# Kernel tuning notes

Measured on AMD Instinct MI355X. Metric: run time of the kernel, lower is better.

## Reference

```python
import jax, jax.numpy as jnp
import numpy as np

N, E, B = 50000, 600000, 64


def setup_inputs() -> dict:
    key = jax.random.key(0)
    ks = jax.random.split(key, 24)
    gn = lambda k, shape, s=0.1: jax.random.normal(k, shape, dtype=jnp.float32) * s
    return {
        "x": gn(ks[0], (N, 1), 1.0),
        "edge_index": jax.random.randint(ks[1], (2, E), 0, N),
        "batch": jnp.sort(jax.random.randint(ks[2], (N,), 0, B)),
        # GATConv(1,128)
        "W1": gn(ks[3], (1, 128)), "a1s": gn(ks[4], (128,)), "a1d": gn(ks[5], (128,)), "b1": jnp.zeros((128,), jnp.float32),
        # GATConv(128,128) x2
        "W2": gn(ks[6], (128, 128)), "a2s": gn(ks[7], (128,)), "a2d": gn(ks[8], (128,)), "b2": jnp.zeros((128,), jnp.float32),
        "W3": gn(ks[9], (128, 128)), "a3s": gn(ks[10], (128,)), "a3d": gn(ks[11], (128,)), "b3": jnp.zeros((128,), jnp.float32),
        # GCNConv(128,64), GCNConv(64,32)
        "Wg1": gn(ks[12], (128, 64)), "bg1": jnp.zeros((64,), jnp.float32),
        "Wg2": gn(ks[13], (64, 32)), "bg2": jnp.zeros((32,), jnp.float32),
        # SoftmaxAggregation learnable temperature (init 1.0)
        "t": jnp.ones((), jnp.float32),
        # Linear heads
        "Wl1": gn(ks[14], (32, 16)), "bl1": jnp.zeros((16,), jnp.float32),
        "Wl2": gn(ks[15], (16, 2)), "bl2": jnp.zeros((2,), jnp.float32),
    }


def reference(x, edge_index, batch, W1, a1s, a1d, b1, W2, a2s, a2d, b2,
              W3, a3s, a3d, b3, Wg1, bg1, Wg2, bg2, t, Wl1, bl1, Wl2, bl2):
    # add self-loops (PyG default for GATConv and GCNConv)
    loops = jnp.arange(N)
    ei = jnp.concatenate([edge_index, jnp.stack([loops, loops])], axis=1)
    src, dst = ei[0], ei[1]  # messages flow src -> dst

    def seg_softmax(logits, seg, num):
        m = jax.ops.segment_max(logits, seg, num)
        m = jnp.where(jnp.isfinite(m), m, 0.0)
        e = jnp.exp(logits - m[seg])
        s = jax.ops.segment_sum(e, seg, num)
        return e / (s[seg] + 1e-16)

    def gat(h_in, W, a_src, a_dst, b):
        h = h_in @ W                                   # [N, F]
        logit = jax.nn.leaky_relu((h @ a_src)[src] + (h @ a_dst)[dst], 0.2)
        alpha = seg_softmax(logit, dst, N)             # edge-softmax over neighbors of dst
        return jax.ops.segment_sum(alpha[:, None] * h[src], dst, N) + b

    def gcn(h_in, W, b):
        deg = jax.ops.segment_sum(jnp.ones(src.shape[0], h_in.dtype), dst, N)
        dinv = jnp.where(deg > 0, jax.lax.rsqrt(deg), 0.0)
        norm = dinv[src] * dinv[dst]                   # symmetric normalization
        h = h_in @ W
        return jax.ops.segment_sum(norm[:, None] * h[src], dst, N) + b

    h = jax.nn.elu(gat(x, W1, a1s, a1d, b1))
    h = jax.nn.elu(gat(h, W2, a2s, a2d, b2))
    h = jax.nn.elu(gat(h, W3, a3s, a3d, b3))
    h = jax.nn.elu(gcn(h, Wg1, bg1))
    h = jax.nn.elu(gcn(h, Wg2, bg2))

    # SoftmaxAggregation: per-graph, per-channel softmax weights w = softmax(t*h)
    logits = h * t
    m = jax.ops.segment_max(logits, batch, B)
    m = jnp.where(jnp.isfinite(m), m, 0.0)
    e = jnp.exp(logits - m[batch])
    s = jax.ops.segment_sum(e, batch, B)
    w = e / (s[batch] + 1e-16)
    g = jax.ops.segment_sum(w * h, batch, B)           # [B, 32]

    g = jax.nn.elu(g @ Wl1 + bl1)
    return jax.nn.log_softmax(g @ Wl2 + bl2, axis=1)
```

## Files before the change

kernel.cpp:

```cpp
#include <hip/hip_runtime.h>
#include <math.h>

static inline int cdiv(long a, long b){ return (int)((a + b - 1) / b); }
static inline char* alignp(char* p, size_t a){ return (char*)(((uintptr_t)p + a - 1) & ~(uintptr_t)(a - 1)); }

typedef __attribute__((ext_vector_type(8))) short bf16x8;
typedef __attribute__((ext_vector_type(4))) short bf16x4;
typedef __attribute__((ext_vector_type(4))) float f32x4;

__device__ __forceinline__ float lrelu(float x){ return x > 0.f ? x : 0.2f * x; }
__device__ __forceinline__ float eluf(float x){ return x > 0.f ? x : __expf(x) - 1.f; }
__device__ __forceinline__ short f2bf(float f){
  unsigned u = __float_as_uint(f);
  return (short)((u + 0x7FFFu + ((u >> 16) & 1u)) >> 16);
}
__device__ __forceinline__ float bflo(unsigned v){ return __uint_as_float(v << 16); }
__device__ __forceinline__ float bfhi(unsigned v){ return __uint_as_float(v & 0xFFFF0000u); }

template<int K, int FOUT, bool DOTS>
__global__ void k_gemm_mfma(const short* __restrict__ Abf, const short* __restrict__ Wp,
                            short* __restrict__ outb,
                            const float* __restrict__ av_s, const float* __restrict__ av_d,
                            float* __restrict__ as_, float* __restrict__ ad_, int N){
  constexpr int NKS = K / 32, NCT = FOUT / 16;
  int wid  = threadIdx.x >> 6;
  int lane = threadIdx.x & 63;
  int rowbase = (blockIdx.x * 4 + wid) * 16;
  if(rowbase >= N) return;
  int arow = rowbase + (lane & 15);
  if(arow >= N) arow = N - 1;
  f32x4 acc[NCT] = {};
  const short* ap = Abf + (long)arow * K + (lane >> 4) * 8;
  #pragma unroll
  for(int ks = 0; ks < NKS; ++ks){
    bf16x8 a = *(const bf16x8*)(ap + ks * 32);
    #pragma unroll
    for(int ct = 0; ct < NCT; ++ct){
      bf16x8 b = *(const bf16x8*)(Wp + ((ks * NCT + ct) * 64 + lane) * 8);
      acc[ct] = __builtin_amdgcn_mfma_f32_16x16x32_bf16(a, b, acc[ct], 0, 0, 0);
    }
  }
  int r0 = rowbase + (lane >> 4) * 4;
  int c0 = lane & 15;
  #pragma unroll
  for(int j = 0; j < 4; ++j){
    int r = r0 + j;
    if(r < N){
      #pragma unroll
      for(int ct = 0; ct < NCT; ++ct)
        outb[(long)r * FOUT + ct * 16 + c0] = f2bf(acc[ct][j]);
    }
  }
  if(DOTS){
    float avs[NCT], avd[NCT];
    #pragma unroll
    for(int ct = 0; ct < NCT; ++ct){ avs[ct] = av_s[ct * 16 + c0]; avd[ct] = av_d[ct * 16 + c0]; }
    #pragma unroll
    for(int j = 0; j < 4; ++j){
      float ps = 0.f, pd = 0.f;
      #pragma unroll
      for(int ct = 0; ct < NCT; ++ct){
        float hv = acc[ct][j];
        ps = fmaf(hv, avs[ct], ps);
        pd = fmaf(hv, avd[ct], pd);
      }
      #pragma unroll
      for(int off = 1; off < 16; off <<= 1){
        ps += __shfl_xor(ps, off);
        pd += __shfl_xor(pd, off);
      }
      int r = r0 + j;
      if(c0 == 0 && r < N){ as_[r] = ps; ad_[r] = pd; }
    }
  }
}

template<int K, int FOUT>
__global__ void k_pack_w(const float* __restrict__ W, short* __restrict__ Wp){
  constexpr int NKS = K / 32, NCT = FOUT / 16;
  int idx = blockIdx.x * blockDim.x + threadIdx.x;
  if(idx >= NKS * NCT * 64) return;
  int lane = idx & 63;
  int ct = (idx >> 6) % NCT;
  int ks = (idx >> 6) / NCT;
  int col = ct * 16 + (lane & 15);
  int kb  = ks * 32 + (lane >> 4) * 8;
  #pragma unroll
  for(int j = 0; j < 8; ++j) Wp[idx * 8 + j] = f2bf(W[(kb + j) * FOUT + col]);
}

__global__ void k_dot128(const float* __restrict__ W1, const float* __restrict__ a1s,
                         const float* __restrict__ a1d, float* __restrict__ S){
  __shared__ float s1[128], s2[128];
  int t = threadIdx.x;
  float w = W1[t];
  s1[t] = w * a1s[t]; s2[t] = w * a1d[t];
  __syncthreads();
  for(int off = 64; off > 0; off >>= 1){
    if(t < off){ s1[t] += s1[t + off]; s2[t] += s2[t + off]; }
    __syncthreads();
  }
  if(t == 0){ S[0] = s1[0]; S[1] = s2[0]; }
}
__global__ void k_l1v(const float* __restrict__ x, const float* __restrict__ W1,
                      short* __restrict__ outb, int N){
  long idx = (long)blockIdx.x * blockDim.x + threadIdx.x;
  if(idx >= (long)N * 16) return;
  int node = (int)(idx >> 4), j8 = ((int)idx & 15) * 8;
  float xv = x[node];
  float4 w0 = *(const float4*)(W1 + j8);
  float4 w1 = *(const float4*)(W1 + j8 + 4);
  bf16x8 v;
  v[0] = f2bf(xv * w0.x); v[1] = f2bf(xv * w0.y);
  v[2] = f2bf(xv * w0.z); v[3] = f2bf(xv * w0.w);
  v[4] = f2bf(xv * w1.x); v[5] = f2bf(xv * w1.y);
  v[6] = f2bf(xv * w1.z); v[7] = f2bf(xv * w1.w);
  *(bf16x8*)(outb + (long)node * 128 + j8) = v;
}
__global__ void k_l1dots(const float* __restrict__ x, const float* __restrict__ S,
                         float* __restrict__ as_, float* __restrict__ ad_, int N){
  int i = blockIdx.x * blockDim.x + threadIdx.x;
  if(i >= N) return;
  float xv = x[i];
  as_[i] = xv * S[0]; ad_[i] = xv * S[1];
}

__global__ void k_deg_init(int* __restrict__ deg, int N){
  int i = blockIdx.x * blockDim.x + threadIdx.x;
  if(i < N) deg[i] = 1;
}
__global__ void k_deg_count8(const int* __restrict__ ei, int E, int Pdiv,
                             int* __restrict__ deg){
  int p = blockIdx.x & 7;
  int lo = p * Pdiv, hi = lo + Pdiv;
  long stride = (long)(gridDim.x >> 3) * blockDim.x;
  for(long e = (long)(blockIdx.x >> 3) * blockDim.x + threadIdx.x; e < E; e += stride){
    int d = ei[E + e];
    if(d >= lo && d < hi) atomicAdd(&deg[d], 1);
  }
}

__global__ void k_scan_part(const int* __restrict__ deg, int* __restrict__ bsum, int N){
  __shared__ int red[256];
  int i = blockIdx.x * 256 + threadIdx.x;
  int v = (i < N) ? deg[i] : 0;
  red[threadIdx.x] = v;
  __syncthreads();
  #pragma unroll
  for(int off = 128; off > 0; off >>= 1){
    if(threadIdx.x < off) red[threadIdx.x] += red[threadIdx.x + off];
    __syncthreads();
  }
  if(threadIdx.x == 0) bsum[blockIdx.x] = red[0];
}
__global__ void k_scan_mid(int* __restrict__ bsum, int NB, int* __restrict__ rowptr, int N){
  __shared__ int buf[1024];
  int t = threadIdx.x;
  int v = (t < NB) ? bsum[t] : 0;
  buf[t] = v;
  __syncthreads();
  for(int off = 1; off < 1024; off <<= 1){
    int u = (t >= off) ? buf[t - off] : 0;
    __syncthreads();
    buf[t] += u;
    __syncthreads();
  }
  if(t < NB) bsum[t] = buf[t] - v;
  if(t == 1023) rowptr[N] = buf[1023];
}
__global__ void k_scan_fin(const int* __restrict__ deg, const int* __restrict__ bsum,
                           int* __restrict__ rowptr, int* __restrict__ cursor,
                           float* __restrict__ dinv, int N){
  __shared__ int buf[256];
  int i = blockIdx.x * 256 + threadIdx.x;
  int t = threadIdx.x;
  int v = (i < N) ? deg[i] : 0;
  buf[t] = v;
  __syncthreads();
  #pragma unroll
  for(int off = 1; off < 256; off <<= 1){
    int u = (t >= off) ? buf[t - off] : 0;
    __syncthreads();
    buf[t] += u;
    __syncthreads();
  }
  if(i < N){
    int ex = buf[t] - v + bsum[blockIdx.x];
    rowptr[i] = ex; cursor[i] = ex;
    dinv[i] = rsqrtf((float)v);
  }
}

__global__ void k_fill8(const int* __restrict__ ei, int E, int N, int Pdiv,
                        int* __restrict__ cursor, int* __restrict__ csr){
  int p = blockIdx.x & 7;
  int lo = p * Pdiv, hi = lo + Pdiv;
  long ET = (long)E + N;
  long stride = (long)(gridDim.x >> 3) * blockDim.x;
  for(long e = (long)(blockIdx.x >> 3) * blockDim.x + threadIdx.x; e < ET; e += stride){
    int d = (e < E) ? ei[E + e] : (int)(e - E);
    if(d < lo || d >= hi) continue;
    int s = (e < E) ? ei[e] : d;
    int pos = atomicAdd(&cursor[d], 1);
    csr[pos] = s;
  }
}

__global__ void k_gat_agg(const int* __restrict__ rowptr, const int* __restrict__ csr,
                          const float* __restrict__ as_, const float* __restrict__ ad_,
                          const short* __restrict__ h, const float* __restrict__ bias,
                          short* __restrict__ out, int N){
  int w = (int)(((long)blockIdx.x * blockDim.x + threadIdx.x) >> 6);
  int lane = threadIdx.x & 63;
  if(w >= N) return;
  int start = rowptr[w], end = rowptr[w + 1];
  int deg = end - start;
  float add = ad_[w];

  int s_reg = 0;
  float alpha_reg = 0.f, m, inv;
  if(deg <= 64){
    float logit = -INFINITY;
    if(lane < deg){
      s_reg = csr[start + lane];
      logit = lrelu(as_[s_reg] + add);
    }
    m = logit;
    #pragma unroll
    for(int off = 32; off > 0; off >>= 1) m = fmaxf(m, __shfl_xor(m, off));
    float e = __expf(logit - m);
    float ssum = e;
    #pragma unroll
    for(int off = 32; off > 0; off >>= 1) ssum += __shfl_xor(ssum, off);
    inv = 1.f / (ssum + 1e-16f);
    alpha_reg = e * inv;
  }else{
    float logit = -INFINITY, ssum = 0.f;
    m = -INFINITY;
    if(lane < deg){
      s_reg = csr[start + lane];
      logit = lrelu(as_[s_reg] + add);
      m = logit; ssum = 1.f;
      for(int e = start + lane + 64; e < end; e += 64){
        int s = csr[e];
        float l = lrelu(as_[s] + add);
        if(l > m){ ssum = ssum * __expf(m - l) + 1.f; m = l; }
        else       ssum += __expf(l - m);
      }
    }
    #pragma unroll
    for(int off = 32; off > 0; off >>= 1){
      float mo = __shfl_xor(m, off);
      float so = __shfl_xor(ssum, off);
      float mn = fmaxf(m, mo);
      float ea = (m  > -INFINITY) ? __expf(m  - mn) : 0.f;
      float eb = (mo > -INFINITY) ? __expf(mo - mn) : 0.f;
      ssum = ssum * ea + so * eb;
      m = mn;
    }
    inv = 1.f / (ssum + 1e-16f);
    alpha_reg = __expf(logit - m) * inv;
  }

  float acc[8] = {};
  int nb = deg < 64 ? deg : 64;
  int g  = lane >> 4;
  int fo = (lane & 15) * 8;
  const short* hf = h + fo;
  for(int k = 0; k < nb; k += 4){
    int idx = k + g;
    if(idx < nb){
      float a = __shfl(alpha_reg, idx);
      int s   = __shfl(s_reg, idx);
      uint4 hv = *(const uint4*)(hf + (long)s * 128);
      acc[0] = fmaf(a, bflo(hv.x), acc[0]);
      acc[1] = fmaf(a, bfhi(hv.x), acc[1]);
      acc[2] = fmaf(a, bflo(hv.y), acc[2]);
      acc[3] = fmaf(a, bfhi(hv.y), acc[3]);
      acc[4] = fmaf(a, bflo(hv.z), acc[4]);
      acc[5] = fmaf(a, bfhi(hv.z), acc[5]);
      acc[6] = fmaf(a, bflo(hv.w), acc[6]);
      acc[7] = fmaf(a, bfhi(hv.w), acc[7]);
    }
  }
  for(int e = start + 64; e < end; ++e){
    if(lane < 16){
      int s = csr[e];
      float l = lrelu(as_[s] + add);
      float a = __expf(l - m) * inv;
      uint4 hv = *(const uint4*)(hf + (long)s * 128);
      acc[0] = fmaf(a, bflo(hv.x), acc[0]);
      acc[1] = fmaf(a, bfhi(hv.x), acc[1]);
      acc[2] = fmaf(a, bflo(hv.y), acc[2]);
      acc[3] = fmaf(a, bfhi(hv.y), acc[3]);
      acc[4] = fmaf(a, bflo(hv.z), acc[4]);
      acc[5] = fmaf(a, bfhi(hv.z), acc[5]);
      acc[6] = fmaf(a, bflo(hv.w), acc[6]);
      acc[7] = fmaf(a, bfhi(hv.w), acc[7]);
    }
  }
  #pragma unroll
  for(int j = 0; j < 8; ++j){
    acc[j] += __shfl_xor(acc[j], 16);
    acc[j] += __shfl_xor(acc[j], 32);
  }
  if(lane < 16){
    float4 b0 = *(const float4*)(bias + fo);
    float4 b1 = *(const float4*)(bias + fo + 4);
    bf16x8 v;
    v[0] = f2bf(eluf(acc[0] + b0.x)); v[1] = f2bf(eluf(acc[1] + b0.y));
    v[2] = f2bf(eluf(acc[2] + b0.z)); v[3] = f2bf(eluf(acc[3] + b0.w));
    v[4] = f2bf(eluf(acc[4] + b1.x)); v[5] = f2bf(eluf(acc[5] + b1.y));
    v[6] = f2bf(eluf(acc[6] + b1.z)); v[7] = f2bf(eluf(acc[7] + b1.w));
    *(bf16x8*)(out + (long)w * 128 + fo) = v;
  }
}

template<int F, bool BFOUT>
__global__ void k_gcn_agg(const int* __restrict__ rowptr, const int* __restrict__ csr,
                          const float* __restrict__ dinv, const short* __restrict__ h,
                          const float* __restrict__ bias, short* __restrict__ out_bf,
                          float* __restrict__ out_f, int N){
  constexpr int FPL = F / 16;
  int w = (int)(((long)blockIdx.x * blockDim.x + threadIdx.x) >> 6);
  int lane = threadIdx.x & 63;
  if(w >= N) return;
  int start = rowptr[w], end = rowptr[w + 1];
  int deg = end - start;
  float dd = dinv[w];
  int s_reg = 0; float dv_reg = 0.f;
  if(lane < deg){
    s_reg = csr[start + lane];
    dv_reg = dinv[s_reg];
  }
  float acc[FPL] = {};
  int nb = deg < 64 ? deg : 64;
  int g  = lane >> 4;
  int fo = (lane & 15) * FPL;
  const short* hf = h + fo;
  for(int k = 0; k < nb; k += 4){
    int idx = k + g;
    if(idx < nb){
      int s = __shfl(s_reg, idx);
      float nrm = dd * __shfl(dv_reg, idx);
      if(FPL == 4){
        uint2 hv = *(const uint2*)(hf + (long)s * F);
        acc[0] = fmaf(nrm, bflo(hv.x), acc[0]);
        acc[1] = fmaf(nrm, bfhi(hv.x), acc[1]);
        acc[2] = fmaf(nrm, bflo(hv.y), acc[2]);
        acc[3] = fmaf(nrm, bfhi(hv.y), acc[3]);
      }else{
        unsigned hv = *(const unsigned*)(hf + (long)s * F);
        acc[0] = fmaf(nrm, bflo(hv), acc[0]);
        acc[1] = fmaf(nrm, bfhi(hv), acc[1]);
      }
    }
  }
  for(int e = start + 64; e < end; ++e){
    if(lane < 16){
      int s = csr[e];
      float nrm = dd * dinv[s];
      if(FPL == 4){
        uint2 hv = *(const uint2*)(hf + (long)s * F);
        acc[0] = fmaf(nrm, bflo(hv.x), acc[0]);
        acc[1] = fmaf(nrm, bfhi(hv.x), acc[1]);
        acc[2] = fmaf(nrm, bflo(hv.y), acc[2]);
        acc[3] = fmaf(nrm, bfhi(hv.y), acc[3]);
      }else{
        unsigned hv = *(const unsigned*)(hf + (long)s * F);
        acc[0] = fmaf(nrm, bflo(hv), acc[0]);
        acc[1] = fmaf(nrm, bfhi(hv), acc[1]);
      }
    }
  }
  #pragma unroll
  for(int j = 0; j < FPL; ++j){
    acc[j] += __shfl_xor(acc[j], 16);
    acc[j] += __shfl_xor(acc[j], 32);
  }
  if(lane < 16){
    if(BFOUT){
      if(FPL == 4){
        bf16x4 v;
        #pragma unroll
        for(int j = 0; j < 4; ++j) v[j] = f2bf(eluf(acc[j] + bias[fo + j]));
        *(bf16x4*)(out_bf + (long)w * F + fo) = v;
      }else{
        #pragma unroll
        for(int j = 0; j < FPL; ++j)
          out_bf[(long)w * F + fo + j] = f2bf(eluf(acc[j] + bias[fo + j]));
      }
    }else{
      if(FPL == 2){
        float2 v2 = make_float2(eluf(acc[0] + bias[fo]), eluf(acc[1] + bias[fo + 1]));
        *(float2*)(out_f + (long)w * F + fo) = v2;
      }else{
        #pragma unroll
        for(int j = 0; j < FPL; ++j)
          out_f[(long)w * F + fo + j] = eluf(acc[j] + bias[fo + j]);
      }
    }
  }
}

template<int S>
__global__ void k_bagg_part(const float* __restrict__ h, const int* __restrict__ batch,
                            const float* __restrict__ t, float* __restrict__ pM,
                            float* __restrict__ pS, float* __restrict__ pV, int N){
  int chunk = blockIdx.x;
  int b = chunk / S, s = chunk % S;
  __shared__ int s_lo, s_hi;
  if(threadIdx.x == 0){
    int lo = 0, hi = N;
    while(lo < hi){ int mid = (lo + hi) >> 1; if(batch[mid] < b) lo = mid + 1; else hi = mid; }
    s_lo = lo;
    int lo2 = lo, hi2 = N;
    while(lo2 < hi2){ int mid = (lo2 + hi2) >> 1; if(batch[mid] < b + 1) lo2 = mid + 1; else hi2 = mid; }
    s_hi = lo2;
  }
  __syncthreads();
  int lo = s_lo, hi = s_hi;
  int len = hi - lo;
  int per = (len + S - 1) / S;
  int clo = lo + s * per;
  int chi = clo + per; if(chi > hi) chi = hi;
  float tv = t[0];
  int c = threadIdx.x & 31, r = threadIdx.x >> 5;

  float m = -INFINITY, ss = 0.f, vv = 0.f;
  for(int i = clo + r; i < chi; i += 8){
    float hv = h[(long)i * 32 + c];
    float l = hv * tv;
    if(l > m){
      float e = (m > -INFINITY) ? __expf(m - l) : 0.f;
      ss = ss * e + 1.f; vv = vv * e + hv; m = l;
    }else{
      float e = __expf(l - m);
      ss += e; vv += e * hv;
    }
  }
  __shared__ float rm[8][32], rs[8][32], rv[8][32];
  rm[r][c] = m; rs[r][c] = ss; rv[r][c] = vv;
  __syncthreads();
  if(r == 0){
    float M = rm[0][c], SS = rs[0][c], VV = rv[0][c];
    #pragma unroll
    for(int k = 1; k < 8; ++k){
      float mo = rm[k][c], so = rs[k][c], vo = rv[k][c];
      float mn = fmaxf(M, mo);
      float ea = (M  > -INFINITY) ? __expf(M  - mn) : 0.f;
      float eb = (mo > -INFINITY) ? __expf(mo - mn) : 0.f;
      SS = SS * ea + so * eb; VV = VV * ea + vo * eb; M = mn;
    }
    pM[chunk * 32 + c] = M; pS[chunk * 32 + c] = SS; pV[chunk * 32 + c] = VV;
  }
}
template<int S>
__global__ void k_bagg_comb(const float* __restrict__ pM, const float* __restrict__ pS,
                            const float* __restrict__ pV, float* __restrict__ g, int B){
  int idx = blockIdx.x * blockDim.x + threadIdx.x;
  if(idx >= B * 32) return;
  int b = idx >> 5, c = idx & 31;
  float M = -INFINITY, SS = 0.f, VV = 0.f;
  #pragma unroll 4
  for(int k = 0; k < S; ++k){
    int p = (b * S + k) * 32 + c;
    float mo = pM[p], so = pS[p], vo = pV[p];
    float mn = fmaxf(M, mo);
    float ea = (M  > -INFINITY) ? __expf(M  - mn) : 0.f;
    float eb = (mo > -INFINITY) ? __expf(mo - mn) : 0.f;
    SS = SS * ea + so * eb; VV = VV * ea + vo * eb; M = mn;
  }
  g[idx] = VV / (SS + 1e-16f);
}

__global__ void k_head(const float* __restrict__ g, const float* __restrict__ Wl1,
                       const float* __restrict__ bl1, const float* __restrict__ Wl2,
                       const float* __restrict__ bl2, float* __restrict__ out, int B){
  int b = blockIdx.x * blockDim.x + threadIdx.x;
  if(b >= B) return;
  float gr[32];
  #pragma unroll
  for(int k = 0; k < 32; ++k) gr[k] = g[b * 32 + k];
  float h1[16];
  #pragma unroll
  for(int j = 0; j < 16; ++j){
    float acc = bl1[j];
    #pragma unroll
    for(int k = 0; k < 32; ++k) acc = fmaf(gr[k], Wl1[k * 16 + j], acc);
    h1[j] = eluf(acc);
  }
  float l0 = bl2[0], l1 = bl2[1];
  #pragma unroll
  for(int k = 0; k < 16; ++k){
    l0 = fmaf(h1[k], Wl2[k * 2 + 0], l0);
    l1 = fmaf(h1[k], Wl2[k * 2 + 1], l1);
  }
  float mx = fmaxf(l0, l1);
  float lse = mx + __logf(__expf(l0 - mx) + __expf(l1 - mx));
  out[b * 2 + 0] = l0 - lse;
  out[b * 2 + 1] = l1 - lse;
}

extern "C" void kernel_launch(void* const* d_in, const int* in_sizes, int n_in,
                              void* d_out, int out_size, void* d_ws, size_t ws_size,
                              hipStream_t stream){
  const float* x     = (const float*)d_in[0];
  const int*   ei    = (const int*)d_in[1];
  const int*   batch = (const int*)d_in[2];
  const float* W1 = (const float*)d_in[3];
  const float* a1s = (const float*)d_in[4];
  const float* a1d = (const float*)d_in[5];
  const float* b1 = (const float*)d_in[6];
  const float* W2 = (const float*)d_in[7];
  const float* a2s = (const float*)d_in[8];
  const float* a2d = (const float*)d_in[9];
  const float* b2 = (const float*)d_in[10];
  const float* W3 = (const float*)d_in[11];
  const float* a3s = (const float*)d_in[12];
  const float* a3d = (const float*)d_in[13];
  const float* b3 = (const float*)d_in[14];
  const float* Wg1 = (const float*)d_in[15];
  const float* bg1 = (const float*)d_in[16];
  const float* Wg2 = (const float*)d_in[17];
  const float* bg2 = (const float*)d_in[18];
  const float* t   = (const float*)d_in[19];
  const float* Wl1 = (const float*)d_in[20];
  const float* bl1 = (const float*)d_in[21];
  const float* Wl2 = (const float*)d_in[22];
  const float* bl2 = (const float*)d_in[23];

  const int N = in_sizes[0];
  const int E = in_sizes[1] / 2;
  const int B = out_size / 2;
  const int ET = E + N;
  float* out = (float*)d_out;
  constexpr int BS = 32;

  char* p = (char*)d_ws;
  short* Hbf  = (short*)p;            p += (size_t)N * 128 * 2;
  short* Abf  = (short*)p;            p += (size_t)N * 128 * 2;
  float* A32  = (float*)p;            p += (size_t)N * 32 * 4;
  float* as_  = (float*)p;            p += (size_t)N * 4;
  float* ad_  = (float*)p;            p += (size_t)N * 4;
  float* dinv = (float*)p;            p += (size_t)N * 4;
  int*   deg    = (int*)p;            p += (size_t)N * 4;
  int*   rowptr = (int*)p;            p += (size_t)(N + 1) * 4;
  int*   cursor = (int*)p;            p += (size_t)N * 4;
  int*   csr    = (int*)p;            p += (size_t)ET * 4;
  int*   bsum   = (int*)p;            p += (size_t)1024 * 4;
  p = alignp(p, 16);
  short* Wp2  = (short*)p;            p += 128 * 128 * 2;
  short* Wp3  = (short*)p;            p += 128 * 128 * 2;
  short* Wpg1 = (short*)p;            p += 128 * 64 * 2;
  short* Wpg2 = (short*)p;            p += 64 * 32 * 2;
  p = alignp(p, 16);
  float* S    = (float*)p;            p += 16 * 4;
  float* pM   = (float*)p;            p += (size_t)B * BS * 32 * 4;
  float* pSb  = (float*)p;            p += (size_t)B * BS * 32 * 4;
  float* pV   = (float*)p;            p += (size_t)B * BS * 32 * 4;
  float* g    = (float*)p;

  const int T = 256;
  const int gN  = cdiv(N, T);
  const int gW  = cdiv((long)N * 64, T);
  const int gG  = cdiv(N, 64);
  const int NB  = cdiv(N, 256);
  const int Pdiv = cdiv(N, 8);

  k_deg_init<<<dim3(gN), dim3(T), 0, stream>>>(deg, N);
  k_deg_count8<<<dim3(2048), dim3(T), 0, stream>>>(ei, E, Pdiv, deg);
  k_scan_part<<<dim3(NB), dim3(256), 0, stream>>>(deg, bsum, N);
  k_scan_mid<<<dim3(1), dim3(1024), 0, stream>>>(bsum, NB, rowptr, N);
  k_scan_fin<<<dim3(NB), dim3(256), 0, stream>>>(deg, bsum, rowptr, cursor, dinv, N);
  k_fill8<<<dim3(2048), dim3(T), 0, stream>>>(ei, E, N, Pdiv, cursor, csr);
  k_pack_w<128,128><<<dim3(8), dim3(T), 0, stream>>>(W2, Wp2);
  k_pack_w<128,128><<<dim3(8), dim3(T), 0, stream>>>(W3, Wp3);
  k_pack_w<128, 64><<<dim3(4), dim3(T), 0, stream>>>(Wg1, Wpg1);
  k_pack_w< 64, 32><<<dim3(1), dim3(T), 0, stream>>>(Wg2, Wpg2);
  k_dot128<<<dim3(1), dim3(128), 0, stream>>>(W1, a1s, a1d, S);

  k_l1v<<<dim3(cdiv((long)N * 16, T)), dim3(T), 0, stream>>>(x, W1, Hbf, N);
  k_l1dots<<<dim3(gN), dim3(T), 0, stream>>>(x, S, as_, ad_, N);
  k_gat_agg<<<dim3(gW), dim3(T), 0, stream>>>(rowptr, csr, as_, ad_, Hbf, b1, Abf, N);

  k_gemm_mfma<128,128,true><<<dim3(gG), dim3(T), 0, stream>>>(Abf, Wp2, Hbf, a2s, a2d, as_, ad_, N);
  k_gat_agg<<<dim3(gW), dim3(T), 0, stream>>>(rowptr, csr, as_, ad_, Hbf, b2, Abf, N);

  k_gemm_mfma<128,128,true><<<dim3(gG), dim3(T), 0, stream>>>(Abf, Wp3, Hbf, a3s, a3d, as_, ad_, N);
  k_gat_agg<<<dim3(gW), dim3(T), 0, stream>>>(rowptr, csr, as_, ad_, Hbf, b3, Abf, N);

  k_gemm_mfma<128,64,false><<<dim3(gG), dim3(T), 0, stream>>>(Abf, Wpg1, Hbf, nullptr, nullptr, nullptr, nullptr, N);
  k_gcn_agg<64,true><<<dim3(gW), dim3(T), 0, stream>>>(rowptr, csr, dinv, Hbf, bg1, Abf, (float*)nullptr, N);

  k_gemm_mfma<64,32,false><<<dim3(gG), dim3(T), 0, stream>>>(Abf, Wpg2, Hbf, nullptr, nullptr, nullptr, nullptr, N);
  k_gcn_agg<32,false><<<dim3(gW), dim3(T), 0, stream>>>(rowptr, csr, dinv, Hbf, bg2, (short*)nullptr, A32, N);

  k_bagg_part<BS><<<dim3(B * BS), dim3(256), 0, stream>>>(A32, batch, t, pM, pSb, pV, N);
  k_bagg_comb<BS><<<dim3(cdiv(B * 32, 256)), dim3(256), 0, stream>>>(pM, pSb, pV, g, B);

  k_head<<<dim3(cdiv(B, 64)), dim3(64), 0, stream>>>(g, Wl1, bl1, Wl2, bl2, out, B);
}
```

Measured before the change: 307.5 us.

## Process two destination nodes per wavefront in GAT/GCN aggregation; fuse setup kernels

The GAT and GCN aggregation kernels now split each 64-lane wavefront into two 32-lane halves, each handling one destination node, so the grid is halved. The average degree is about 13, which left most lanes idle under one node per wave. Separately, the four weight-packing kernels and the attention-dot kernel are merged into one launch, and the layer-1 dot computation is folded into k_l1v, removing several small launches. Nodes with more than 32 neighbours now fall to the serial tail loop sooner, which costs more on high-degree nodes.

```diff
diff --git a/kernel.cpp b/kernel.cpp
--- a/kernel.cpp
+++ b/kernel.cpp
@@ -76,9 +76,8 @@
 }
 
 template<int K, int FOUT>
-__global__ void k_pack_w(const float* __restrict__ W, short* __restrict__ Wp){
+__device__ __forceinline__ void pack_dev(const float* __restrict__ W, short* __restrict__ Wp, int idx){
   constexpr int NKS = K / 32, NCT = FOUT / 16;
-  int idx = blockIdx.x * blockDim.x + threadIdx.x;
   if(idx >= NKS * NCT * 64) return;
   int lane = idx & 63;
   int ct = (idx >> 6) % NCT;
@@ -88,22 +87,34 @@
   #pragma unroll
   for(int j = 0; j < 8; ++j) Wp[idx * 8 + j] = f2bf(W[(kb + j) * FOUT + col]);
 }
-
-__global__ void k_dot128(const float* __restrict__ W1, const float* __restrict__ a1s,
-                         const float* __restrict__ a1d, float* __restrict__ S){
-  __shared__ float s1[128], s2[128];
-  int t = threadIdx.x;
-  float w = W1[t];
-  s1[t] = w * a1s[t]; s2[t] = w * a1d[t];
-  __syncthreads();
-  for(int off = 64; off > 0; off >>= 1){
-    if(t < off){ s1[t] += s1[t + off]; s2[t] += s2[t + off]; }
+__global__ void k_pack_all(const float* __restrict__ W2, const float* __restrict__ W3,
+                           const float* __restrict__ Wg1, const float* __restrict__ Wg2,
+                           const float* __restrict__ W1, const float* __restrict__ a1s,
+                           const float* __restrict__ a1d,
+                           short* __restrict__ Wp2, short* __restrict__ Wp3,
+                           short* __restrict__ Wpg1, short* __restrict__ Wpg2,
+                           float* __restrict__ S){
+  int b = blockIdx.x;
+  if(b < 8)       pack_dev<128,128>(W2,  Wp2,  b * 256 + threadIdx.x);
+  else if(b < 16) pack_dev<128,128>(W3,  Wp3,  (b - 8) * 256 + threadIdx.x);
+  else if(b < 20) pack_dev<128, 64>(Wg1, Wpg1, (b - 16) * 256 + threadIdx.x);
+  else if(b == 20) pack_dev<64, 32>(Wg2, Wpg2, threadIdx.x);
+  else{
+    __shared__ float s1[128], s2[128];
+    int t = threadIdx.x;
+    if(t < 128){ float w = W1[t]; s1[t] = w * a1s[t]; s2[t] = w * a1d[t]; }
     __syncthreads();
-  }
-  if(t == 0){ S[0] = s1[0]; S[1] = s2[0]; }
-}
+    for(int off = 64; off > 0; off >>= 1){
+      if(t < off){ s1[t] += s1[t + off]; s2[t] += s2[t + off]; }
+      __syncthreads();
+    }
+    if(t == 0){ S[0] = s1[0]; S[1] = s2[0]; }
+  }
+}
+
 __global__ void k_l1v(const float* __restrict__ x, const float* __restrict__ W1,
-                      short* __restrict__ outb, int N){
+                      const float* __restrict__ S, short* __restrict__ outb,
+                      float* __restrict__ as_, float* __restrict__ ad_, int N){
   long idx = (long)blockIdx.x * blockDim.x + threadIdx.x;
   if(idx >= (long)N * 16) return;
   int node = (int)(idx >> 4), j8 = ((int)idx & 15) * 8;
@@ -116,13 +127,7 @@
   v[4] = f2bf(xv * w1.x); v[5] = f2bf(xv * w1.y);
   v[6] = f2bf(xv * w1.z); v[7] = f2bf(xv * w1.w);
   *(bf16x8*)(outb + (long)node * 128 + j8) = v;
-}
-__global__ void k_l1dots(const float* __restrict__ x, const float* __restrict__ S,
-                         float* __restrict__ as_, float* __restrict__ ad_, int N){
-  int i = blockIdx.x * blockDim.x + threadIdx.x;
-  if(i >= N) return;
-  float xv = x[i];
-  as_[i] = xv * S[0]; ad_[i] = xv * S[1];
+  if((idx & 15) == 0){ as_[node] = xv * S[0]; ad_[node] = xv * S[1]; }
 }
 
 __global__ void k_deg_init(int* __restrict__ deg, int N){
@@ -210,68 +215,67 @@
                           const float* __restrict__ as_, const float* __restrict__ ad_,
                           const short* __restrict__ h, const float* __restrict__ bias,
                           short* __restrict__ out, int N){
-  int w = (int)(((long)blockIdx.x * blockDim.x + threadIdx.x) >> 6);
+  int pair = (int)(((long)blockIdx.x * blockDim.x + threadIdx.x) >> 6);
+  if(pair * 2 >= N) return;
   int lane = threadIdx.x & 63;
-  if(w >= N) return;
-  int start = rowptr[w], end = rowptr[w + 1];
-  int deg = end - start;
-  float add = ad_[w];
+  int half = lane >> 5, hl = lane & 31;
+  int w = pair * 2 + half;
+  bool active = (w < N);
+  int start = 0, end = 0, deg = 0;
+  float add = 0.f;
+  if(active){ start = rowptr[w]; end = rowptr[w + 1]; deg = end - start; add = ad_[w]; }
 
   int s_reg = 0;
-  float alpha_reg = 0.f, m, inv;
-  if(deg <= 64){
-    float logit = -INFINITY;
-    if(lane < deg){
-      s_reg = csr[start + lane];
-      logit = lrelu(as_[s_reg] + add);
-    }
+  float logit = -INFINITY;
+  if(hl < deg){
+    s_reg = csr[start + hl];
+    logit = lrelu(as_[s_reg] + add);
+  }
+  float m, inv, alpha_reg;
+  if(deg <= 32){
     m = logit;
     #pragma unroll
-    for(int off = 32; off > 0; off >>= 1) m = fmaxf(m, __shfl_xor(m, off));
+    for(int off = 16; off > 0; off >>= 1) m = fmaxf(m, __shfl_xor(m, off));
     float e = __expf(logit - m);
     float ssum = e;
     #pragma unroll
-    for(int off = 32; off > 0; off >>= 1) ssum += __shfl_xor(ssum, off);
+    for(int off = 16; off > 0; off >>= 1) ssum += __shfl_xor(ssum, off);
     inv = 1.f / (ssum + 1e-16f);
     alpha_reg = e * inv;
   }else{
-    float logit = -INFINITY, ssum = 0.f;
-    m = -INFINITY;
-    if(lane < deg){
-      s_reg = csr[start + lane];
-      logit = lrelu(as_[s_reg] + add);
-      m = logit; ssum = 1.f;
-      for(int e = start + lane + 64; e < end; e += 64){
-        int s = csr[e];
-        float l = lrelu(as_[s] + add);
-        if(l > m){ ssum = ssum * __expf(m - l) + 1.f; m = l; }
-        else       ssum += __expf(l - m);
-      }
-    }
-    #pragma unroll
-    for(int off = 32; off > 0; off >>= 1){
-      float mo = __shfl_xor(m, off);
+    float mm = logit, ssum = (hl < deg) ? 1.f : 0.f;
+    for(int e = start + hl + 32; e < end; e += 32){
+      int s = csr[e];
+      float l = lrelu(as_[s] + add);
+      if(l > mm){ ssum = ssum * __expf(mm - l) + 1.f; mm = l; }
+      else        ssum += __expf(l - mm);
+    }
+    #pragma unroll
+    for(int off = 16; off > 0; off >>= 1){
+      float mo = __shfl_xor(mm, off);
       float so = __shfl_xor(ssum, off);
-      float mn = fmaxf(m, mo);
-      float ea = (m  > -INFINITY) ? __expf(m  - mn) : 0.f;
+      float mn = fmaxf(mm, mo);
+      float ea = (mm > -INFINITY) ? __expf(mm - mn) : 0.f;
       float eb = (mo > -INFINITY) ? __expf(mo - mn) : 0.f;
       ssum = ssum * ea + so * eb;
-      m = mn;
-    }
+      mm = mn;
+    }
+    m = mm;
     inv = 1.f / (ssum + 1e-16f);
     alpha_reg = __expf(logit - m) * inv;
   }
 
   float acc[8] = {};
-  int nb = deg < 64 ? deg : 64;
-  int g  = lane >> 4;
-  int fo = (lane & 15) * 8;
+  int nb = deg < 32 ? deg : 32;
+  int gg = hl >> 4;
+  int fo = (hl & 15) * 8;
   const short* hf = h + fo;
-  for(int k = 0; k < nb; k += 4){
-    int idx = k + g;
+  for(int k = 0; k < nb; k += 2){
+    int idx = k + gg;
     if(idx < nb){
-      float a = __shfl(alpha_reg, idx);
-      int s   = __shfl(s_reg, idx);
+      int sl = (half << 5) + idx;
+      float a = __shfl(alpha_reg, sl);
+      int s   = __shfl(s_reg, sl);
       uint4 hv = *(const uint4*)(hf + (long)s * 128);
       acc[0] = fmaf(a, bflo(hv.x), acc[0]);
       acc[1] = fmaf(a, bfhi(hv.x), acc[1]);
@@ -283,8 +287,8 @@
       acc[7] = fmaf(a, bfhi(hv.w), acc[7]);
     }
   }
-  for(int e = start + 64; e < end; ++e){
-    if(lane < 16){
+  for(int e = start + 32; e < end; ++e){
+    if(hl < 16){
       int s = csr[e];
       float l = lrelu(as_[s] + add);
       float a = __expf(l - m) * inv;
@@ -300,11 +304,8 @@
     }
   }
   #pragma unroll
-  for(int j = 0; j < 8; ++j){
-    acc[j] += __shfl_xor(acc[j], 16);
-    acc[j] += __shfl_xor(acc[j], 32);
-  }
-  if(lane < 16){
+  for(int j = 0; j < 8; ++j) acc[j] += __shfl_xor(acc[j], 16);
+  if(active && hl < 16){
     float4 b0 = *(const float4*)(bias + fo);
     float4 b1 = *(const float4*)(bias + fo + 4);
     bf16x8 v;
@@ -322,27 +323,31 @@
                           const float* __restrict__ bias, short* __restrict__ out_bf,
                           float* __restrict__ out_f, int N){
   constexpr int FPL = F / 16;
-  int w = (int)(((long)blockIdx.x * blockDim.x + threadIdx.x) >> 6);
+  int pair = (int)(((long)blockIdx.x * blockDim.x + threadIdx.x) >> 6);
+  if(pair * 2 >= N) return;
   int lane = threadIdx.x & 63;
-  if(w >= N) return;
-  int start = rowptr[w], end = rowptr[w + 1];
-  int deg = end - start;
-  float dd = dinv[w];
+  int half = lane >> 5, hl = lane & 31;
+  int w = pair * 2 + half;
+  bool active = (w < N);
+  int start = 0, end = 0, deg = 0;
+  float dd = 0.f;
+  if(active){ start = rowptr[w]; end = rowptr[w + 1]; deg = end - start; dd = dinv[w]; }
   int s_reg = 0; float dv_reg = 0.f;
-  if(lane < deg){
-    s_reg = csr[start + lane];
+  if(hl < deg){
+    s_reg = csr[start + hl];
     dv_reg = dinv[s_reg];
   }
   float acc[FPL] = {};
-  int nb = deg < 64 ? deg : 64;
-  int g  = lane >> 4;
-  int fo = (lane & 15) * FPL;
+  int nb = deg < 32 ? deg : 32;
+  int gg = hl >> 4;
+  int fo = (hl & 15) * FPL;
   const short* hf = h + fo;
-  for(int k = 0; k < nb; k += 4){
-    int idx = k + g;
+  for(int k = 0; k < nb; k += 2){
+    int idx = k + gg;
     if(idx < nb){
-      int s = __shfl(s_reg, idx);
-      float nrm = dd * __shfl(dv_reg, idx);
+      int sl = (half << 5) + idx;
+      int s = __shfl(s_reg, sl);
+      float nrm = dd * __shfl(dv_reg, sl);
       if(FPL == 4){
         uint2 hv = *(const uint2*)(hf + (long)s * F);
         acc[0] = fmaf(nrm, bflo(hv.x), acc[0]);
@@ -356,8 +361,8 @@
       }
     }
   }
-  for(int e = start + 64; e < end; ++e){
-    if(lane < 16){
+  for(int e = start + 32; e < end; ++e){
+    if(hl < 16){
       int s = csr[e];
       float nrm = dd * dinv[s];
       if(FPL == 4){
@@ -374,11 +379,8 @@
     }
   }
   #pragma unroll
-  for(int j = 0; j < FPL; ++j){
-    acc[j] += __shfl_xor(acc[j], 16);
-    acc[j] += __shfl_xor(acc[j], 32);
-  }
-  if(lane < 16){
+  for(int j = 0; j < FPL; ++j) acc[j] += __shfl_xor(acc[j], 16);
+  if(active && hl < 16){
     if(BFOUT){
       if(FPL == 4){
         bf16x4 v;
@@ -562,10 +564,10 @@
   float* g    = (float*)p;
 
   const int T = 256;
-  const int gN  = cdiv(N, T);
-  const int gW  = cdiv((long)N * 64, T);
-  const int gG  = cdiv(N, 64);
-  const int NB  = cdiv(N, 256);
+  const int gN   = cdiv(N, T);
+  const int gW2  = cdiv((long)N * 32, T);
+  const int gG   = cdiv(N, 64);
+  const int NB   = cdiv(N, 256);
   const int Pdiv = cdiv(N, 8);
 
   k_deg_init<<<dim3(gN), dim3(T), 0, stream>>>(deg, N);
@@ -574,27 +576,23 @@
   k_scan_mid<<<dim3(1), dim3(1024), 0, stream>>>(bsum, NB, rowptr, N);
   k_scan_fin<<<dim3(NB), dim3(256), 0, stream>>>(deg, bsum, rowptr, cursor, dinv, N);
   k_fill8<<<dim3(2048), dim3(T), 0, stream>>>(ei, E, N, Pdiv, cursor, csr);
-  k_pack_w<128,128><<<dim3(8), dim3(T), 0, stream>>>(W2, Wp2);
-  k_pack_w<128,128><<<dim3(8), dim3(T), 0, stream>>>(W3, Wp3);
-  k_pack_w<128, 64><<<dim3(4), dim3(T), 0, stream>>>(Wg1, Wpg1);
-  k_pack_w< 64, 32><<<dim3(1), dim3(T), 0, stream>>>(Wg2, Wpg2);
-  k_dot128<<<dim3(1), dim3(128), 0, stream>>>(W1, a1s, a1d, S);
-
-  k_l1v<<<dim3(cdiv((long)N * 16, T)), dim3(T), 0, stream>>>(x, W1, Hbf, N);
-  k_l1dots<<<dim3(gN), dim3(T), 0, stream>>>(x, S, as_, ad_, N);
-  k_gat_agg<<<dim3(gW), dim3(T), 0, stream>>>(rowptr, csr, as_, ad_, Hbf, b1, Abf, N);
+  k_pack_all<<<dim3(22), dim3(T), 0, stream>>>(W2, W3, Wg1, Wg2, W1, a1s, a1d,
+                                               Wp2, Wp3, Wpg1, Wpg2, S);
+
+  k_l1v<<<dim3(cdiv((long)N * 16, T)), dim3(T), 0, stream>>>(x, W1, S, Hbf, as_, ad_, N);
+  k_gat_agg<<<dim3(gW2), dim3(T), 0, stream>>>(rowptr, csr, as_, ad_, Hbf, b1, Abf, N);
 
   k_gemm_mfma<128,128,true><<<dim3(gG), dim3(T), 0, stream>>>(Abf, Wp2, Hbf, a2s, a2d, as_, ad_, N);
-  k_gat_agg<<<dim3(gW), dim3(T), 0, stream>>>(rowptr, csr, as_, ad_, Hbf, b2, Abf, N);
+  k_gat_agg<<<dim3(gW2), dim3(T), 0, stream>>>(rowptr, csr, as_, ad_, Hbf, b2, Abf, N);
 
   k_gemm_mfma<128,128,true><<<dim3(gG), dim3(T), 0, stream>>>(Abf, Wp3, Hbf, a3s, a3d, as_, ad_, N);
-  k_gat_agg<<<dim3(gW), dim3(T), 0, stream>>>(rowptr, csr, as_, ad_, Hbf, b3, Abf, N);
+  k_gat_agg<<<dim3(gW2), dim3(T), 0, stream>>>(rowptr, csr, as_, ad_, Hbf, b3, Abf, N);
 
   k_gemm_mfma<128,64,false><<<dim3(gG), dim3(T), 0, stream>>>(Abf, Wpg1, Hbf, nullptr, nullptr, nullptr, nullptr, N);
-  k_gcn_agg<64,true><<<dim3(gW), dim3(T), 0, stream>>>(rowptr, csr, dinv, Hbf, bg1, Abf, (float*)nullptr, N);
+  k_gcn_agg<64,true><<<dim3(gW2), dim3(T), 0, stream>>>(rowptr, csr, dinv, Hbf, bg1, Abf, (float*)nullptr, N);
 
   k_gemm_mfma<64,32,false><<<dim3(gG), dim3(T), 0, stream>>>(Abf, Wpg2, Hbf, nullptr, nullptr, nullptr, nullptr, N);
-  k_gcn_agg<32,false><<<dim3(gW), dim3(T), 0, stream>>>(rowptr, csr, dinv, Hbf, bg2, (short*)nullptr, A32, N);
+  k_gcn_agg<32,false><<<dim3(gW2), dim3(T), 0, stream>>>(rowptr, csr, dinv, Hbf, bg2, (short*)nullptr, A32, N);
 
   k_bagg_part<BS><<<dim3(B * BS), dim3(256), 0, stream>>>(A32, batch, t, pM, pSb, pV, N);
   k_bagg_comb<BS><<<dim3(cdiv(B * 32, 256)), dim3(256), 0, stream>>>(pM, pSb, pV, g, B);
```

New measurement: 278.4 us. 1.1x faster.
